# Performance work log

Measured on AMD Instinct MI355X. Metric: run time of the kernel, lower is better.

## Reference

```python
import jax, jax.numpy as jnp
import numpy as np

W_SZ = 7
SHIFT = 3
HEADS = 6
DIM = 192
HID = 4 * DIM
B, H, W = 16, 112, 112


def _rel_index(w):
    ch = np.arange(w)
    coords = np.stack(np.meshgrid(ch, ch, indexing='ij')).reshape(2, -1)  # (2, w*w)
    rel = coords[:, :, None] - coords[:, None, :]
    rel = rel.transpose(1, 2, 0).copy()
    rel[:, :, 0] += w - 1
    rel[:, :, 1] += w - 1
    rel[:, :, 0] *= 2 * w - 1
    return jnp.asarray(rel.sum(-1))  # (w*w, w*w) int

REL_IDX = _rel_index(W_SZ)


def _make_attn_mask(Hh, Ww, w, s):
    img = np.zeros((Hh, Ww), dtype=np.float32)
    cnt = 0
    sls = (slice(0, -w), slice(-w, -s), slice(-s, None))
    for hs in sls:
        for ws in sls:
            img[hs, ws] = cnt
            cnt += 1
    nH, nW = Hh // w, Ww // w
    mw = img.reshape(nH, w, nW, w).transpose(0, 2, 1, 3).reshape(-1, w * w)
    mask = np.where(mw[:, None, :] != mw[:, :, None], -100.0, 0.0).astype(np.float32)
    return jnp.asarray(mask)  # (nW_total, N, N)


def _ln(x, g, b):
    m = x.mean(-1, keepdims=True)
    v = ((x - m) ** 2).mean(-1, keepdims=True)
    return (x - m) / jnp.sqrt(v + 1e-5) * g + b


def setup_inputs() -> dict:
    key = jax.random.key(0)
    ks = jax.random.split(key, 16)
    C, hid = DIM, HID
    p = lambda k, shape: (jax.random.normal(k, shape, dtype=jnp.float32) * 0.02)
    return {
        'x': jax.random.normal(ks[0], (B, H, W, C), dtype=jnp.float32),
        'attn_mask': _make_attn_mask(H, W, W_SZ, SHIFT),
        'norm1_g': jnp.ones((C,), jnp.float32),
        'norm1_b': jnp.zeros((C,), jnp.float32),
        'qkv_w': p(ks[1], (C, 3 * C)),
        'qkv_b': jnp.zeros((3 * C,), jnp.float32),
        'rpb': p(ks[2], ((2 * W_SZ - 1) * (2 * W_SZ - 1), HEADS)),
        'proj_w': p(ks[3], (C, C)),
        'proj_b': jnp.zeros((C,), jnp.float32),
        'norm2_g': jnp.ones((C,), jnp.float32),
        'norm2_b': jnp.zeros((C,), jnp.float32),
        'fc1_w': p(ks[4], (C, hid)),
        'fc1_b': jnp.zeros((hid,), jnp.float32),
        'fc2_w': p(ks[5], (hid, C)),
        'fc2_b': jnp.zeros((C,), jnp.float32),
    }


def reference(x, attn_mask, norm1_g, norm1_b, qkv_w, qkv_b, rpb, proj_w, proj_b,
              norm2_g, norm2_b, fc1_w, fc1_b, fc2_w, fc2_b):
    Bb, Hh, Ww, C = x.shape
    w, s, h = W_SZ, SHIFT, HEADS
    d = C // h
    N = w * w
    nH, nW = Hh // w, Ww // w
    nWin = nH * nW

    shortcut = x
    xn = _ln(x, norm1_g, norm1_b)
    # cyclic shift
    xs = jnp.roll(xn, (-s, -s), axis=(1, 2))
    # window partition -> (B*nWin, N, C)
    xw = xs.reshape(Bb, nH, w, nW, w, C).transpose(0, 1, 3, 2, 4, 5).reshape(Bb * nWin, N, C)

    qkv = (xw @ qkv_w + qkv_b).reshape(-1, N, 3, h, d).transpose(2, 0, 3, 1, 4)
    q, k, v = qkv[0] * (d ** -0.5), qkv[1], qkv[2]  # (B_, h, N, d)
    attn = jnp.einsum('bhnd,bhmd->bhnm', q, k)
    bias = rpb[REL_IDX].transpose(2, 0, 1)  # (h, N, N)
    attn = attn + bias[None]
    attn = attn.reshape(Bb, nWin, h, N, N) + attn_mask[None, :, None]
    attn = jax.nn.softmax(attn.reshape(-1, h, N, N), axis=-1)
    out = jnp.einsum('bhnm,bhmd->bhnd', attn, v).transpose(0, 2, 1, 3).reshape(-1, N, C)
    out = out @ proj_w + proj_b

    # window reverse + reverse shift
    out = out.reshape(Bb, nH, nW, w, w, C).transpose(0, 1, 3, 2, 4, 5).reshape(Bb, Hh, Ww, C)
    out = jnp.roll(out, (s, s), axis=(1, 2))

    x2 = shortcut + out
    y = _ln(x2, norm2_g, norm2_b)
    y = jax.nn.gelu(y @ fc1_w + fc1_b, approximate=False) @ fc2_w + fc2_b
    return x2 + y
```

## Files before the change

### kernel.cpp

```cpp
#include <hip/hip_runtime.h>
#include <hip/hip_bf16.h>
#include <math.h>

typedef __hip_bfloat16 bf16;
typedef __attribute__((ext_vector_type(8))) __bf16 bf16x8;
typedef __attribute__((ext_vector_type(4))) float f32x4;

#define DIM 192
#define N 49
#define HEADS 6
#define TOKENS 200704
#define NWIN_TOT 4096

__device__ __forceinline__ float b2f(bf16 v) { return __bfloat162float(v); }
__device__ __forceinline__ bf16 f2b(float v) { return __float2bfloat16(v); }
__device__ __forceinline__ unsigned short f2bu(float f) {
    union { bf16 b; unsigned short u; } cv; cv.b = __float2bfloat16(f); return cv.u;
}
__device__ __forceinline__ float u2f(unsigned short u) {
    return __uint_as_float(((unsigned int)u) << 16);
}
__device__ __forceinline__ bool is_fp32(const unsigned int* detect) {
    return detect[0] == 0x3F800000u;
}

__device__ __forceinline__ int swz_sx(int t, int b) {
    return (t * 384 + b) ^ ((t & 7) << 4);
}
__device__ __forceinline__ int swz64(int row, int b) {
    return (row * 64 + b) ^ (((row >> 1) & 3) << 4);
}
__device__ __forceinline__ int swz128(int row, int b) {
    return (row * 128 + b) ^ ((row & 7) << 4);
}

struct ConvArgs {
    const void* src[14];
    bf16* dst[14];
    int sz[14];
    const unsigned int* detect;
    int total;
};

__global__ __launch_bounds__(256) void k_convert(ConvArgs a) {
    bool f32 = is_fp32(a.detect);
    for (int g = blockIdx.x * 256 + threadIdx.x; g < a.total; g += gridDim.x * 256) {
        int i = g, b = 0;
        while (i >= a.sz[b]) { i -= a.sz[b]; ++b; }
        float v = f32 ? ((const float*)a.src[b])[i]
                      : b2f(((const bf16*)a.src[b])[i]);
        a.dst[b][i] = f2b(v);
    }
}

__global__ __launch_bounds__(256) void k_transpose(
    const bf16* __restrict__ w1, const bf16* __restrict__ w2,
    const bf16* __restrict__ qw, const bf16* __restrict__ pw,
    bf16* __restrict__ w1t, bf16* __restrict__ w2t,
    bf16* __restrict__ qwt, bf16* __restrict__ pwt)
{
    int i = blockIdx.x * 256 + threadIdx.x;
    if (i < 192 * 768) {
        int k = i / 768, n = i % 768;
        w1t[n * 192 + k] = w1[i];
        int k2 = i / 192, n2 = i % 192;
        w2t[n2 * 768 + k2] = w2[i];
    }
    if (i < 192 * 576) {
        int k = i / 576, n = i % 576;
        qwt[n * 192 + k] = qw[i];
    }
    if (i < 192 * 192) {
        int k = i / 192, n = i % 192;
        pwt[n * 192 + k] = pw[i];
    }
}

__global__ __launch_bounds__(256, 2) void k_attn(
    const void* __restrict__ x, const unsigned int* __restrict__ detect,
    const bf16* __restrict__ n1g, const bf16* __restrict__ n1b,
    const bf16* __restrict__ qwt, const bf16* __restrict__ qkv_b,
    const bf16* __restrict__ rpb, const bf16* __restrict__ pwt,
    const bf16* __restrict__ pb, float* __restrict__ x2out)
{
    __shared__ __align__(16) unsigned short sx[64 * 192];
    __shared__ __align__(16) unsigned short sq[64 * 32];
    __shared__ __align__(16) unsigned short sk[64 * 32];
    __shared__ __align__(16) unsigned short svt[32 * 64];
    __shared__ __align__(16) unsigned short sp[64 * 64];
    __shared__ __align__(16) unsigned short so[64 * 32];
    __shared__ unsigned short srpb[169 * 6 + 2];
    __shared__ unsigned short sqb[576];
    __shared__ float sm[N], sr[N];

    const int tid = threadIdx.x, wi = blockIdx.x;
    const int b = wi >> 8, win = wi & 255;
    const int wv = tid >> 6, ln = tid & 63;
    const int tr = ln & 15, kg = ln >> 4;
    const int wrow = wv * 16;
    const int tloc = wrow + tr;
    const bool f32 = is_fp32(detect);
    char* sxc = (char*)sx;
    char* sqc = (char*)sq;
    char* skc = (char*)sk;
    char* svtc = (char*)svt;
    char* spc = (char*)sp;
    char* soc = (char*)so;

    for (int i = tid; i < 169 * 6; i += 256) srpb[i] = ((const unsigned short*)rpb)[i];
    for (int i = tid; i < 576; i += 256) sqb[i] = ((const unsigned short*)qkv_b)[i];

    for (int t = wv; t < N; t += 4) {
        int ip = (win >> 4) * 7 + t / 7;
        int jp = (win & 15) * 7 + t % 7;
        int si = ip + 3; if (si >= 112) si -= 112;
        int sj = jp + 3; if (sj >= 112) sj -= 112;
        size_t base = (size_t)((b * 112 + si) * 112 + sj) * DIM;
        float v0, v1, v2;
        if (f32) {
            const float* s = (const float*)x + base;
            v0 = s[ln]; v1 = s[ln + 64]; v2 = s[ln + 128];
        } else {
            const bf16* s = (const bf16*)x + base;
            v0 = b2f(s[ln]); v1 = b2f(s[ln + 64]); v2 = b2f(s[ln + 128]);
        }
        float s1 = v0 + v1 + v2, s2 = v0 * v0 + v1 * v1 + v2 * v2;
#pragma unroll
        for (int o = 32; o; o >>= 1) { s1 += __shfl_xor(s1, o, 64); s2 += __shfl_xor(s2, o, 64); }
        if (ln == 0) {
            float m = s1 * (1.f / 192.f);
            sm[t] = m;
            sr[t] = rsqrtf(s2 * (1.f / 192.f) - m * m + 1e-5f);
        }
    }
    __syncthreads();

    for (int i = tid; i < 64 * 192; i += 256) {
        int t = i / 192, c = i - t * 192;
        float v = 0.f;
        if (t < N) {
            int ip = (win >> 4) * 7 + t / 7;
            int jp = (win & 15) * 7 + t % 7;
            int si = ip + 3; if (si >= 112) si -= 112;
            int sj = jp + 3; if (sj >= 112) sj -= 112;
            size_t base = (size_t)((b * 112 + si) * 112 + sj) * DIM + c;
            float xv = f32 ? ((const float*)x)[base] : b2f(((const bf16*)x)[base]);
            v = (xv - sm[t]) * sr[t] * b2f(n1g[c]) + b2f(n1b[c]);
        }
        *(unsigned short*)(sxc + swz_sx(t, c * 2)) = f2bu(v);
    }

    int ridx_[4][4];
    float base_[4][4];
    {
        const int wr = win >> 4, wc = win & 15;
#pragma unroll
        for (int r = 0; r < 4; ++r) {
            int n = wrow + kg * 4 + r;
            int ni = n / 7, nj = n % 7;
            int regrn = (wr == 15) ? (ni >= 4 ? 2 : 1) : 0;
            int regcn = (wc == 15) ? (nj >= 4 ? 2 : 1) : 0;
#pragma unroll
            for (int mt = 0; mt < 4; ++mt) {
                int m = mt * 16 + tr;
                if (m >= N || n >= N) {
                    base_[r][mt] = -1e4f;
                    ridx_[r][mt] = 0;
                } else {
                    int mi = m / 7, mj = m % 7;
                    int regrm = (wr == 15) ? (mi >= 4 ? 2 : 1) : 0;
                    int regcm = (wc == 15) ? (mj >= 4 ? 2 : 1) : 0;
                    base_[r][mt] = (regrn != regrm || regcn != regcm) ? -100.f : 0.f;
                    ridx_[r][mt] = (ni - mi + 6) * 13 + (nj - mj + 6);
                }
            }
        }
    }

    f32x4 yacc[12];
#pragma unroll
    for (int nt = 0; nt < 12; ++nt) yacc[nt] = (f32x4){0.f, 0.f, 0.f, 0.f};

    __syncthreads();

    for (int h = 0; h < HEADS; ++h) {
        f32x4 qa[6];
#pragma unroll
        for (int nt = 0; nt < 6; ++nt) qa[nt] = (f32x4){0.f, 0.f, 0.f, 0.f};
#pragma unroll
        for (int ks = 0; ks < 6; ++ks) {
            bf16x8 a = *(const bf16x8*)(sxc + swz_sx(tloc, ks * 64 + kg * 16));
#pragma unroll
            for (int nt = 0; nt < 6; ++nt) {
                int ncol = (nt >> 1) * 192 + h * 32 + (nt & 1) * 16 + tr;
                bf16x8 bb = *(const bf16x8*)((const char*)qwt + (size_t)ncol * 384 + ks * 64 + kg * 16);
                qa[nt] = __builtin_amdgcn_mfma_f32_16x16x32_bf16(a, bb, qa[nt], 0, 0, 0);
            }
        }
#pragma unroll
        for (int nt = 0; nt < 6; ++nt) {
            const int which = nt >> 1;
            const int dloc = (nt & 1) * 16 + tr;
            const float bias = u2f(sqb[which * 192 + h * 32 + dloc]);
#pragma unroll
            for (int r = 0; r < 4; ++r) {
                const int t = wrow + kg * 4 + r;
                float v = qa[nt][r] + bias;
                if (which == 0) {
                    v *= 0.17677669529663687f;
                    *(unsigned short*)(sqc + swz64(t, dloc * 2)) = f2bu(v);
                } else if (which == 1) {
                    *(unsigned short*)(skc + swz64(t, dloc * 2)) = f2bu(v);
                } else {
                    *(unsigned short*)(svtc + swz128(dloc, t * 2)) = f2bu(v);
                }
            }
        }
        __syncthreads();

        f32x4 s4[4];
        {
            bf16x8 aq = *(const bf16x8*)(sqc + swz64(tloc, kg * 16));
#pragma unroll
            for (int mt = 0; mt < 4; ++mt) {
                bf16x8 bk = *(const bf16x8*)(skc + swz64(mt * 16 + tr, kg * 16));
                s4[mt] = __builtin_amdgcn_mfma_f32_16x16x32_bf16(
                    aq, bk, (f32x4){0.f, 0.f, 0.f, 0.f}, 0, 0, 0);
            }
        }
        float p[4][4];
#pragma unroll
        for (int mt = 0; mt < 4; ++mt)
#pragma unroll
            for (int r = 0; r < 4; ++r)
                p[mt][r] = s4[mt][r] + base_[r][mt] + u2f(srpb[ridx_[r][mt] * 6 + h]);
#pragma unroll
        for (int r = 0; r < 4; ++r) {
            float mx = fmaxf(fmaxf(p[0][r], p[1][r]), fmaxf(p[2][r], p[3][r]));
            mx = fmaxf(mx, __shfl_xor(mx, 1, 64));
            mx = fmaxf(mx, __shfl_xor(mx, 2, 64));
            mx = fmaxf(mx, __shfl_xor(mx, 4, 64));
            mx = fmaxf(mx, __shfl_xor(mx, 8, 64));
            float s = 0.f;
#pragma unroll
            for (int mt = 0; mt < 4; ++mt) { p[mt][r] = __expf(p[mt][r] - mx); s += p[mt][r]; }
            s += __shfl_xor(s, 1, 64);
            s += __shfl_xor(s, 2, 64);
            s += __shfl_xor(s, 4, 64);
            s += __shfl_xor(s, 8, 64);
            float inv = 1.f / s;
#pragma unroll
            for (int mt = 0; mt < 4; ++mt) p[mt][r] *= inv;
        }
#pragma unroll
        for (int mt = 0; mt < 4; ++mt)
#pragma unroll
            for (int r = 0; r < 4; ++r)
                *(unsigned short*)(spc + swz128(wrow + kg * 4 + r, (mt * 16 + tr) * 2)) = f2bu(p[mt][r]);
        __syncthreads();

        f32x4 oacc[2];
#pragma unroll
        for (int nt = 0; nt < 2; ++nt) oacc[nt] = (f32x4){0.f, 0.f, 0.f, 0.f};
#pragma unroll
        for (int ks = 0; ks < 2; ++ks) {
            bf16x8 ap = *(const bf16x8*)(spc + swz128(tloc, ks * 64 + kg * 16));
#pragma unroll
            for (int nt = 0; nt < 2; ++nt) {
                bf16x8 bv = *(const bf16x8*)(svtc + swz128(nt * 16 + tr, ks * 64 + kg * 16));
                oacc[nt] = __builtin_amdgcn_mfma_f32_16x16x32_bf16(ap, bv, oacc[nt], 0, 0, 0);
            }
        }
#pragma unroll
        for (int nt = 0; nt < 2; ++nt)
#pragma unroll
            for (int r = 0; r < 4; ++r)
                *(unsigned short*)(soc + swz64(wrow + kg * 4 + r, (nt * 16 + tr) * 2)) = f2bu(oacc[nt][r]);
        __syncthreads();

        {
            bf16x8 ao = *(const bf16x8*)(soc + swz64(tloc, kg * 16));
#pragma unroll
            for (int nt = 0; nt < 12; ++nt) {
                bf16x8 bp = *(const bf16x8*)((const char*)pwt + (size_t)(nt * 16 + tr) * 384 + h * 64 + kg * 16);
                yacc[nt] = __builtin_amdgcn_mfma_f32_16x16x32_bf16(ao, bp, yacc[nt], 0, 0, 0);
            }
        }
        __syncthreads();
    }

#pragma unroll
    for (int r = 0; r < 4; ++r) {
        const int n = wrow + kg * 4 + r;
        if (n >= N) continue;
        int ip = (win >> 4) * 7 + n / 7;
        int jp = (win & 15) * 7 + n % 7;
        int oi = ip + 3; if (oi >= 112) oi -= 112;
        int oj = jp + 3; if (oj >= 112) oj -= 112;
        const size_t base = (size_t)((b * 112 + oi) * 112 + oj) * DIM;
#pragma unroll
        for (int nt = 0; nt < 12; ++nt) {
            const int col = nt * 16 + tr;
            float xres = f32 ? ((const float*)x)[base + col]
                             : b2f(((const bf16*)x)[base + col]);
            x2out[base + col] = yacc[nt][r] + b2f(pb[col]) + xres;
        }
    }
}

__global__ __launch_bounds__(512, 2) void k_mlp(
    const bf16* __restrict__ n2g, const bf16* __restrict__ n2b,
    const bf16* __restrict__ w1t, const bf16* __restrict__ b1,
    const bf16* __restrict__ w2t, const bf16* __restrict__ b2v,
    float* __restrict__ io)
{
    __shared__ __align__(16) unsigned short sA[128 * 192];
    __shared__ __align__(16) unsigned short sW1[64 * 192];
    __shared__ __align__(16) unsigned short sW2[192 * 64];
    __shared__ __align__(16) unsigned short sH[128 * 64];

    const int tid = threadIdx.x;
    const int ln = tid & 63;
    const int wv = tid >> 6;
    const int tr = ln & 15;
    const int kg = ln >> 4;
    const int wtok = wv * 16;
    char* sAc = (char*)sA;
    char* sW1c = (char*)sW1;
    char* sW2c = (char*)sW2;
    char* sHc = (char*)sH;
    const size_t tbase = (size_t)blockIdx.x * 128;

    {
        const int tok = tid >> 2;
        const int cb = (tid & 3) * 48;
        const float* src = io + (tbase + tok) * 192 + cb;
        float xr[48];
#pragma unroll
        for (int i = 0; i < 12; ++i) {
            float4 v = *(const float4*)(src + i * 4);
            xr[i * 4 + 0] = v.x; xr[i * 4 + 1] = v.y;
            xr[i * 4 + 2] = v.z; xr[i * 4 + 3] = v.w;
        }
        float s1 = 0.f, s2 = 0.f;
#pragma unroll
        for (int i = 0; i < 48; ++i) { s1 += xr[i]; s2 += xr[i] * xr[i]; }
        s1 += __shfl_xor(s1, 1, 64); s2 += __shfl_xor(s2, 1, 64);
        s1 += __shfl_xor(s1, 2, 64); s2 += __shfl_xor(s2, 2, 64);
        const float m = s1 * (1.f / 192.f);
        const float rinv = rsqrtf(s2 * (1.f / 192.f) - m * m + 1e-5f);
        const int tswz = (tok & 7) << 4;
#pragma unroll
        for (int c8 = 0; c8 < 6; ++c8) {
            unsigned short us[8];
#pragma unroll
            for (int j = 0; j < 8; ++j) {
                int c = cb + c8 * 8 + j;
                us[j] = f2bu((xr[c8 * 8 + j] - m) * rinv * b2f(n2g[c]) + b2f(n2b[c]));
            }
            uint4 pv;
            pv.x = (unsigned)us[0] | ((unsigned)us[1] << 16);
            pv.y = (unsigned)us[2] | ((unsigned)us[3] << 16);
            pv.z = (unsigned)us[4] | ((unsigned)us[5] << 16);
            pv.w = (unsigned)us[6] | ((unsigned)us[7] << 16);
            *(uint4*)(sAc + ((tok * 384 + (cb + c8 * 8) * 2) ^ tswz)) = pv;
        }
    }

    f32x4 yacc[12];
#pragma unroll
    for (int ct = 0; ct < 12; ++ct) yacc[ct] = (f32x4){0.f, 0.f, 0.f, 0.f};

    const int arow = wtok + tr;
    const int aswz = (arow & 7) << 4;

    uint4 p1[3], p2[3];
#pragma unroll
    for (int i = 0; i < 3; ++i) {
        int u = tid + i * 512;
        p1[i] = *(const uint4*)((const char*)w1t + (size_t)u * 16);
        int c = u >> 3, o = (u & 7) * 16;
        p2[i] = *(const uint4*)((const char*)w2t + (size_t)c * 1536 + o);
    }

    for (int ch = 0; ch < 12; ++ch) {
        __syncthreads();
#pragma unroll
        for (int i = 0; i < 3; ++i) {
            int u = tid + i * 512;
            int n = u / 24, no = (u % 24) * 16;
            *(uint4*)(sW1c + ((n * 384 + no) ^ ((n & 7) << 4))) = p1[i];
            int c = u >> 3, o = (u & 7) * 16;
            *(uint4*)(sW2c + ((c * 128 + o) ^ ((c & 7) << 4))) = p2[i];
        }
        __syncthreads();
        if (ch + 1 < 12) {
#pragma unroll
            for (int i = 0; i < 3; ++i) {
                int u = tid + i * 512;
                p1[i] = *(const uint4*)((const char*)w1t + (size_t)(ch + 1) * 24576 + (size_t)u * 16);
                int c = u >> 3, o = (u & 7) * 16;
                p2[i] = *(const uint4*)((const char*)w2t + (size_t)c * 1536 + (size_t)(ch + 1) * 128 + o);
            }
        }

        f32x4 hacc[4];
#pragma unroll
        for (int nt = 0; nt < 4; ++nt) hacc[nt] = (f32x4){0.f, 0.f, 0.f, 0.f};
#pragma unroll
        for (int kk = 0; kk < 6; ++kk) {
            const int k0b = (kk * 32 + kg * 8) * 2;
            bf16x8 afrag = *(const bf16x8*)(sAc + ((arow * 384 + k0b) ^ aswz));
#pragma unroll
            for (int nt = 0; nt < 4; ++nt) {
                const int n = nt * 16 + tr;
                bf16x8 bfrag = *(const bf16x8*)(sW1c + ((n * 384 + k0b) ^ ((n & 7) << 4)));
                hacc[nt] = __builtin_amdgcn_mfma_f32_16x16x32_bf16(afrag, bfrag, hacc[nt], 0, 0, 0);
            }
        }

#pragma unroll
        for (int nt = 0; nt < 4; ++nt) {
            const int col = nt * 16 + tr;
            const float bb = b2f(b1[ch * 64 + col]);
#pragma unroll
            for (int r = 0; r < 4; ++r) {
                const int row = wtok + kg * 4 + r;
                float v = hacc[nt][r] + bb;
                float ge = 0.5f * v * (1.f + erff(v * 0.70710678118654752f));
                *(unsigned short*)(sHc + ((row * 128 + col * 2) ^ ((row & 7) << 4))) = f2bu(ge);
            }
        }

#pragma unroll
        for (int kk = 0; kk < 2; ++kk) {
            const int k0b = (kk * 32 + kg * 8) * 2;
            bf16x8 afrag = *(const bf16x8*)(sHc + ((arow * 128 + k0b) ^ aswz));
#pragma unroll
            for (int ct = 0; ct < 12; ++ct) {
                const int c = ct * 16 + tr;
                bf16x8 bfrag = *(const bf16x8*)(sW2c + ((c * 128 + k0b) ^ ((c & 7) << 4)));
                yacc[ct] = __builtin_amdgcn_mfma_f32_16x16x32_bf16(afrag, bfrag, yacc[ct], 0, 0, 0);
            }
        }
    }

#pragma unroll
    for (int ct = 0; ct < 12; ++ct) {
        const int col = ct * 16 + tr;
        const float bb = b2f(b2v[col]);
#pragma unroll
        for (int r = 0; r < 4; ++r) {
            const size_t gi = (tbase + wtok + kg * 4 + r) * 192 + col;
            io[gi] += yacc[ct][r] + bb;
        }
    }
}

extern "C" void kernel_launch(void* const* d_in, const int* in_sizes, int n_in,
                              void* d_out, int out_size, void* d_ws, size_t ws_size,
                              hipStream_t stream) {
    const void* x = d_in[0];
    const unsigned int* detect = (const unsigned int*)d_in[2];
    float* out = (float*)d_out;

    bf16* conv = (bf16*)d_ws;
    ConvArgs ca;
    int total = 0;
    size_t off = 0;
    for (int i = 0; i < 14; i++) {
        int sz = in_sizes[i + 1];
        ca.src[i] = d_in[i + 1];
        ca.dst[i] = conv + off;
        ca.sz[i] = sz;
        off += (size_t)((sz + 7) & ~7);
        total += sz;
    }
    ca.detect = detect;
    ca.total = total;

    bf16* n1g = ca.dst[1],  *n1b = ca.dst[2];
    bf16* qkvw = ca.dst[3], *qkvb = ca.dst[4];
    bf16* rpb = ca.dst[5];
    bf16* pw = ca.dst[6],   *pb = ca.dst[7];
    bf16* n2g = ca.dst[8],  *n2b = ca.dst[9];
    bf16* w1 = ca.dst[10],  *b1 = ca.dst[11];
    bf16* w2 = ca.dst[12],  *b2v = ca.dst[13];

    bf16* w1t = conv + off;
    bf16* w2t = w1t + 192 * 768;
    bf16* qwt = w2t + 192 * 768;
    bf16* pwt = qwt + 192 * 576;

    k_convert<<<1024, 256, 0, stream>>>(ca);
    k_transpose<<<576, 256, 0, stream>>>(w1, w2, qkvw, pw, w1t, w2t, qwt, pwt);
    k_attn<<<NWIN_TOT, 256, 0, stream>>>(x, detect, n1g, n1b, qwt, qkvb,
                                         rpb, pwt, pb, out);
    k_mlp<<<TOKENS / 128, 512, 0, stream>>>(n2g, n2b, w1t, b1, w2t, b2v, out);
}
```

Before: 1.451 ms.

## Process head pairs per iteration and split QKV/proj GEMMs across waves by column

The attention kernel now handles two heads per loop iteration. The QKV and output-projection GEMMs are re-partitioned so each wave owns a slice of output columns across all 64 rows, instead of owning a 16-row slice and reloading every weight column. This cuts redundant global weight loads per wave and halves the number of head-loop barriers. LayerNorm1 is fused into the statistics pass, with gamma and beta cached in LDS, which removes a second global read of x. In exchange, LDS use rises from the larger q/k/v/p/o buffers, and the 4x3 accumulator arrays add register pressure, either of which could reduce occupancy.

```diff
diff --git a/kernel.cpp b/kernel.cpp
--- a/kernel.cpp
+++ b/kernel.cpp
@@ -26,9 +26,6 @@
 
 __device__ __forceinline__ int swz_sx(int t, int b) {
     return (t * 384 + b) ^ ((t & 7) << 4);
-}
-__device__ __forceinline__ int swz64(int row, int b) {
-    return (row * 64 + b) ^ (((row >> 1) & 3) << 4);
 }
 __device__ __forceinline__ int swz128(int row, int b) {
     return (row * 128 + b) ^ ((row & 7) << 4);
@@ -84,14 +81,14 @@
     const bf16* __restrict__ pb, float* __restrict__ x2out)
 {
     __shared__ __align__(16) unsigned short sx[64 * 192];
-    __shared__ __align__(16) unsigned short sq[64 * 32];
-    __shared__ __align__(16) unsigned short sk[64 * 32];
-    __shared__ __align__(16) unsigned short svt[32 * 64];
-    __shared__ __align__(16) unsigned short sp[64 * 64];
-    __shared__ __align__(16) unsigned short so[64 * 32];
+    __shared__ __align__(16) unsigned short sq[64 * 64];
+    __shared__ __align__(16) unsigned short sk[64 * 64];
+    __shared__ __align__(16) unsigned short svt[64 * 64];
+    __shared__ __align__(16) unsigned short sp2[2 * 64 * 64];
+    __shared__ __align__(16) unsigned short so2[64 * 64];
     __shared__ unsigned short srpb[169 * 6 + 2];
     __shared__ unsigned short sqb[576];
-    __shared__ float sm[N], sr[N];
+    __shared__ unsigned short sg1[192], sb1[192];
 
     const int tid = threadIdx.x, wi = blockIdx.x;
     const int b = wi >> 8, win = wi & 255;
@@ -104,11 +101,14 @@
     char* sqc = (char*)sq;
     char* skc = (char*)sk;
     char* svtc = (char*)svt;
-    char* spc = (char*)sp;
-    char* soc = (char*)so;
+    char* spc = (char*)sp2;
+    char* soc = (char*)so2;
 
     for (int i = tid; i < 169 * 6; i += 256) srpb[i] = ((const unsigned short*)rpb)[i];
     for (int i = tid; i < 576; i += 256) sqb[i] = ((const unsigned short*)qkv_b)[i];
+    if (tid < 192) { sg1[tid] = ((const unsigned short*)n1g)[tid];
+                     sb1[tid] = ((const unsigned short*)n1b)[tid]; }
+    __syncthreads();
 
     for (int t = wv; t < N; t += 4) {
         int ip = (win >> 4) * 7 + t / 7;
@@ -127,27 +127,18 @@
         float s1 = v0 + v1 + v2, s2 = v0 * v0 + v1 * v1 + v2 * v2;
 #pragma unroll
         for (int o = 32; o; o >>= 1) { s1 += __shfl_xor(s1, o, 64); s2 += __shfl_xor(s2, o, 64); }
-        if (ln == 0) {
-            float m = s1 * (1.f / 192.f);
-            sm[t] = m;
-            sr[t] = rsqrtf(s2 * (1.f / 192.f) - m * m + 1e-5f);
-        }
-    }
-    __syncthreads();
-
-    for (int i = tid; i < 64 * 192; i += 256) {
-        int t = i / 192, c = i - t * 192;
-        float v = 0.f;
-        if (t < N) {
-            int ip = (win >> 4) * 7 + t / 7;
-            int jp = (win & 15) * 7 + t % 7;
-            int si = ip + 3; if (si >= 112) si -= 112;
-            int sj = jp + 3; if (sj >= 112) sj -= 112;
-            size_t base = (size_t)((b * 112 + si) * 112 + sj) * DIM + c;
-            float xv = f32 ? ((const float*)x)[base] : b2f(((const bf16*)x)[base]);
-            v = (xv - sm[t]) * sr[t] * b2f(n1g[c]) + b2f(n1b[c]);
-        }
-        *(unsigned short*)(sxc + swz_sx(t, c * 2)) = f2bu(v);
+        const float m = s1 * (1.f / 192.f);
+        const float rinv = rsqrtf(s2 * (1.f / 192.f) - m * m + 1e-5f);
+        *(unsigned short*)(sxc + swz_sx(t, ln * 2)) =
+            f2bu((v0 - m) * rinv * u2f(sg1[ln]) + u2f(sb1[ln]));
+        *(unsigned short*)(sxc + swz_sx(t, (ln + 64) * 2)) =
+            f2bu((v1 - m) * rinv * u2f(sg1[ln + 64]) + u2f(sb1[ln + 64]));
+        *(unsigned short*)(sxc + swz_sx(t, (ln + 128) * 2)) =
+            f2bu((v2 - m) * rinv * u2f(sg1[ln + 128]) + u2f(sb1[ln + 128]));
+    }
+    for (int i = tid; i < 15 * 192; i += 256) {
+        int t = 49 + i / 192, c = i - (i / 192) * 192;
+        *(unsigned short*)(sxc + swz_sx(t, c * 2)) = 0;
     }
 
     int ridx_[4][4];
@@ -177,133 +168,168 @@
         }
     }
 
-    f32x4 yacc[12];
-#pragma unroll
-    for (int nt = 0; nt < 12; ++nt) yacc[nt] = (f32x4){0.f, 0.f, 0.f, 0.f};
+    f32x4 yacc[4][3];
+#pragma unroll
+    for (int mt = 0; mt < 4; ++mt)
+#pragma unroll
+        for (int j = 0; j < 3; ++j) yacc[mt][j] = (f32x4){0.f, 0.f, 0.f, 0.f};
 
     __syncthreads();
 
-    for (int h = 0; h < HEADS; ++h) {
-        f32x4 qa[6];
-#pragma unroll
-        for (int nt = 0; nt < 6; ++nt) qa[nt] = (f32x4){0.f, 0.f, 0.f, 0.f};
+    for (int hp = 0; hp < 3; ++hp) {
+        const int h0 = hp * 2;
+        f32x4 qa[3][4];
+#pragma unroll
+        for (int j = 0; j < 3; ++j)
+#pragma unroll
+            for (int mt = 0; mt < 4; ++mt) qa[j][mt] = (f32x4){0.f, 0.f, 0.f, 0.f};
 #pragma unroll
         for (int ks = 0; ks < 6; ++ks) {
-            bf16x8 a = *(const bf16x8*)(sxc + swz_sx(tloc, ks * 64 + kg * 16));
-#pragma unroll
-            for (int nt = 0; nt < 6; ++nt) {
-                int ncol = (nt >> 1) * 192 + h * 32 + (nt & 1) * 16 + tr;
-                bf16x8 bb = *(const bf16x8*)((const char*)qwt + (size_t)ncol * 384 + ks * 64 + kg * 16);
-                qa[nt] = __builtin_amdgcn_mfma_f32_16x16x32_bf16(a, bb, qa[nt], 0, 0, 0);
-            }
-        }
-#pragma unroll
-        for (int nt = 0; nt < 6; ++nt) {
-            const int which = nt >> 1;
-            const int dloc = (nt & 1) * 16 + tr;
-            const float bias = u2f(sqb[which * 192 + h * 32 + dloc]);
-#pragma unroll
-            for (int r = 0; r < 4; ++r) {
-                const int t = wrow + kg * 4 + r;
-                float v = qa[nt][r] + bias;
-                if (which == 0) {
-                    v *= 0.17677669529663687f;
-                    *(unsigned short*)(sqc + swz64(t, dloc * 2)) = f2bu(v);
-                } else if (which == 1) {
-                    *(unsigned short*)(skc + swz64(t, dloc * 2)) = f2bu(v);
-                } else {
-                    *(unsigned short*)(svtc + swz128(dloc, t * 2)) = f2bu(v);
+            bf16x8 bb[3];
+#pragma unroll
+            for (int j = 0; j < 3; ++j) {
+                int g = wv * 3 + j;
+                int ncol = (g >> 2) * 192 + h0 * 32 + (g & 3) * 16 + tr;
+                bb[j] = *(const bf16x8*)((const char*)qwt + (size_t)ncol * 384 + ks * 64 + kg * 16);
+            }
+#pragma unroll
+            for (int mt = 0; mt < 4; ++mt) {
+                bf16x8 a = *(const bf16x8*)(sxc + swz_sx(mt * 16 + tr, ks * 64 + kg * 16));
+#pragma unroll
+                for (int j = 0; j < 3; ++j)
+                    qa[j][mt] = __builtin_amdgcn_mfma_f32_16x16x32_bf16(a, bb[j], qa[j][mt], 0, 0, 0);
+            }
+        }
+#pragma unroll
+        for (int j = 0; j < 3; ++j) {
+            int g = wv * 3 + j;
+            int s = g >> 2, w16 = (g & 3) * 16;
+            int ncol = s * 192 + h0 * 32 + w16 + tr;
+            float bias = u2f(sqb[ncol]);
+#pragma unroll
+            for (int mt = 0; mt < 4; ++mt) {
+#pragma unroll
+                for (int r = 0; r < 4; ++r) {
+                    int row = mt * 16 + kg * 4 + r;
+                    float v = qa[j][mt][r] + bias;
+                    if (s == 0) {
+                        v *= 0.17677669529663687f;
+                        *(unsigned short*)(sqc + swz128(row, (w16 + tr) * 2)) = f2bu(v);
+                    } else if (s == 1) {
+                        *(unsigned short*)(skc + swz128(row, (w16 + tr) * 2)) = f2bu(v);
+                    } else {
+                        *(unsigned short*)(svtc + swz128(w16 + tr, row * 2)) = f2bu(v);
+                    }
                 }
             }
         }
         __syncthreads();
 
-        f32x4 s4[4];
-        {
-            bf16x8 aq = *(const bf16x8*)(sqc + swz64(tloc, kg * 16));
+#pragma unroll
+        for (int hh = 0; hh < 2; ++hh) {
+            const int h = h0 + hh;
+            f32x4 s4[4];
+            bf16x8 aq = *(const bf16x8*)(sqc + swz128(tloc, hh * 64 + kg * 16));
 #pragma unroll
             for (int mt = 0; mt < 4; ++mt) {
-                bf16x8 bk = *(const bf16x8*)(skc + swz64(mt * 16 + tr, kg * 16));
+                bf16x8 bk = *(const bf16x8*)(skc + swz128(mt * 16 + tr, hh * 64 + kg * 16));
                 s4[mt] = __builtin_amdgcn_mfma_f32_16x16x32_bf16(
                     aq, bk, (f32x4){0.f, 0.f, 0.f, 0.f}, 0, 0, 0);
             }
-        }
-        float p[4][4];
-#pragma unroll
-        for (int mt = 0; mt < 4; ++mt)
-#pragma unroll
-            for (int r = 0; r < 4; ++r)
-                p[mt][r] = s4[mt][r] + base_[r][mt] + u2f(srpb[ridx_[r][mt] * 6 + h]);
+            float p[4][4];
+#pragma unroll
+            for (int mt = 0; mt < 4; ++mt)
+#pragma unroll
+                for (int r = 0; r < 4; ++r)
+                    p[mt][r] = s4[mt][r] + base_[r][mt] + u2f(srpb[ridx_[r][mt] * 6 + h]);
+#pragma unroll
+            for (int r = 0; r < 4; ++r) {
+                float mx = fmaxf(fmaxf(p[0][r], p[1][r]), fmaxf(p[2][r], p[3][r]));
+                mx = fmaxf(mx, __shfl_xor(mx, 1, 64));
+                mx = fmaxf(mx, __shfl_xor(mx, 2, 64));
+                mx = fmaxf(mx, __shfl_xor(mx, 4, 64));
+                mx = fmaxf(mx, __shfl_xor(mx, 8, 64));
+                float s = 0.f;
+#pragma unroll
+                for (int mt = 0; mt < 4; ++mt) { p[mt][r] = __expf(p[mt][r] - mx); s += p[mt][r]; }
+                s += __shfl_xor(s, 1, 64);
+                s += __shfl_xor(s, 2, 64);
+                s += __shfl_xor(s, 4, 64);
+                s += __shfl_xor(s, 8, 64);
+                float inv = 1.f / s;
+#pragma unroll
+                for (int mt = 0; mt < 4; ++mt) p[mt][r] *= inv;
+            }
+#pragma unroll
+            for (int mt = 0; mt < 4; ++mt)
+#pragma unroll
+                for (int r = 0; r < 4; ++r)
+                    *(unsigned short*)(spc + hh * 8192 +
+                        swz128(wrow + kg * 4 + r, (mt * 16 + tr) * 2)) = f2bu(p[mt][r]);
+        }
+        __syncthreads();
+
+#pragma unroll
+        for (int hh = 0; hh < 2; ++hh) {
+            f32x4 oacc[2];
+#pragma unroll
+            for (int nt = 0; nt < 2; ++nt) oacc[nt] = (f32x4){0.f, 0.f, 0.f, 0.f};
+#pragma unroll
+            for (int ks = 0; ks < 2; ++ks) {
+                bf16x8 ap = *(const bf16x8*)(spc + hh * 8192 + swz128(tloc, ks * 64 + kg * 16));
+#pragma unroll
+                for (int nt = 0; nt < 2; ++nt) {
+                    bf16x8 bv = *(const bf16x8*)(svtc + swz128(hh * 32 + nt * 16 + tr, ks * 64 + kg * 16));
+                    oacc[nt] = __builtin_amdgcn_mfma_f32_16x16x32_bf16(ap, bv, oacc[nt], 0, 0, 0);
+                }
+            }
+#pragma unroll
+            for (int nt = 0; nt < 2; ++nt)
+#pragma unroll
+                for (int r = 0; r < 4; ++r)
+                    *(unsigned short*)(soc + swz128(wrow + kg * 4 + r,
+                        (hh * 32 + nt * 16 + tr) * 2)) = f2bu(oacc[nt][r]);
+        }
+        __syncthreads();
+
+#pragma unroll
+        for (int hh = 0; hh < 2; ++hh) {
+            const int h = h0 + hh;
+            bf16x8 bp[3];
+#pragma unroll
+            for (int j = 0; j < 3; ++j) {
+                int ncol = wv * 48 + j * 16 + tr;
+                bp[j] = *(const bf16x8*)((const char*)pwt + (size_t)ncol * 384 + h * 64 + kg * 16);
+            }
+#pragma unroll
+            for (int mt = 0; mt < 4; ++mt) {
+                bf16x8 ao = *(const bf16x8*)(soc + swz128(mt * 16 + tr, hh * 64 + kg * 16));
+#pragma unroll
+                for (int j = 0; j < 3; ++j)
+                    yacc[mt][j] = __builtin_amdgcn_mfma_f32_16x16x32_bf16(ao, bp[j], yacc[mt][j], 0, 0, 0);
+            }
+        }
+        __syncthreads();
+    }
+
+#pragma unroll
+    for (int mt = 0; mt < 4; ++mt) {
 #pragma unroll
         for (int r = 0; r < 4; ++r) {
-            float mx = fmaxf(fmaxf(p[0][r], p[1][r]), fmaxf(p[2][r], p[3][r]));
-            mx = fmaxf(mx, __shfl_xor(mx, 1, 64));
-            mx = fmaxf(mx, __shfl_xor(mx, 2, 64));
-            mx = fmaxf(mx, __shfl_xor(mx, 4, 64));
-            mx = fmaxf(mx, __shfl_xor(mx, 8, 64));
-            float s = 0.f;
-#pragma unroll
-            for (int mt = 0; mt < 4; ++mt) { p[mt][r] = __expf(p[mt][r] - mx); s += p[mt][r]; }
-            s += __shfl_xor(s, 1, 64);
-            s += __shfl_xor(s, 2, 64);
-            s += __shfl_xor(s, 4, 64);
-            s += __shfl_xor(s, 8, 64);
-            float inv = 1.f / s;
-#pragma unroll
-            for (int mt = 0; mt < 4; ++mt) p[mt][r] *= inv;
-        }
-#pragma unroll
-        for (int mt = 0; mt < 4; ++mt)
-#pragma unroll
-            for (int r = 0; r < 4; ++r)
-                *(unsigned short*)(spc + swz128(wrow + kg * 4 + r, (mt * 16 + tr) * 2)) = f2bu(p[mt][r]);
-        __syncthreads();
-
-        f32x4 oacc[2];
-#pragma unroll
-        for (int nt = 0; nt < 2; ++nt) oacc[nt] = (f32x4){0.f, 0.f, 0.f, 0.f};
-#pragma unroll
-        for (int ks = 0; ks < 2; ++ks) {
-            bf16x8 ap = *(const bf16x8*)(spc + swz128(tloc, ks * 64 + kg * 16));
-#pragma unroll
-            for (int nt = 0; nt < 2; ++nt) {
-                bf16x8 bv = *(const bf16x8*)(svtc + swz128(nt * 16 + tr, ks * 64 + kg * 16));
-                oacc[nt] = __builtin_amdgcn_mfma_f32_16x16x32_bf16(ap, bv, oacc[nt], 0, 0, 0);
-            }
-        }
-#pragma unroll
-        for (int nt = 0; nt < 2; ++nt)
-#pragma unroll
-            for (int r = 0; r < 4; ++r)
-                *(unsigned short*)(soc + swz64(wrow + kg * 4 + r, (nt * 16 + tr) * 2)) = f2bu(oacc[nt][r]);
-        __syncthreads();
-
-        {
-            bf16x8 ao = *(const bf16x8*)(soc + swz64(tloc, kg * 16));
-#pragma unroll
-            for (int nt = 0; nt < 12; ++nt) {
-                bf16x8 bp = *(const bf16x8*)((const char*)pwt + (size_t)(nt * 16 + tr) * 384 + h * 64 + kg * 16);
-                yacc[nt] = __builtin_amdgcn_mfma_f32_16x16x32_bf16(ao, bp, yacc[nt], 0, 0, 0);
-            }
-        }
-        __syncthreads();
-    }
-
-#pragma unroll
-    for (int r = 0; r < 4; ++r) {
-        const int n = wrow + kg * 4 + r;
-        if (n >= N) continue;
-        int ip = (win >> 4) * 7 + n / 7;
-        int jp = (win & 15) * 7 + n % 7;
-        int oi = ip + 3; if (oi >= 112) oi -= 112;
-        int oj = jp + 3; if (oj >= 112) oj -= 112;
-        const size_t base = (size_t)((b * 112 + oi) * 112 + oj) * DIM;
-#pragma unroll
-        for (int nt = 0; nt < 12; ++nt) {
-            const int col = nt * 16 + tr;
-            float xres = f32 ? ((const float*)x)[base + col]
-                             : b2f(((const bf16*)x)[base + col]);
-            x2out[base + col] = yacc[nt][r] + b2f(pb[col]) + xres;
+            const int n = mt * 16 + kg * 4 + r;
+            if (n >= N) continue;
+            int ip = (win >> 4) * 7 + n / 7;
+            int jp = (win & 15) * 7 + n % 7;
+            int oi = ip + 3; if (oi >= 112) oi -= 112;
+            int oj = jp + 3; if (oj >= 112) oj -= 112;
+            const size_t base = (size_t)((b * 112 + oi) * 112 + oj) * DIM;
+#pragma unroll
+            for (int j = 0; j < 3; ++j) {
+                const int col = wv * 48 + j * 16 + tr;
+                float xres = f32 ? ((const float*)x)[base + col]
+                                 : b2f(((const bf16*)x)[base + col]);
+                x2out[base + col] = yacc[mt][j][r] + b2f(pb[col]) + xres;
+            }
         }
     }
 }
```

Result: faster. 1.404 ms (-3.2%).
